# Kernel optimization log

Hardware: AMD Instinct MI355X
Metric: run time of the kernel (lower is better)

Reference implementation:

```python
import jax, jax.numpy as jnp
import numpy as np

N_NODES = 100000
N_EDGES = 3200000
N_GRAPHS = 32
D_IN = 128
D_HID = 128
N_CLASSES = 10


def setup_inputs() -> dict:
    key = jax.random.key(0)
    ks = jax.random.split(key, 16)
    h = jax.random.normal(ks[0], (N_NODES, D_IN), dtype=jnp.float32)
    src = jax.random.randint(ks[1], (N_EDGES,), 0, N_NODES, dtype=jnp.int32)
    dst = jax.random.randint(ks[2], (N_EDGES,), 0, N_NODES, dtype=jnp.int32)
    graph_ids = jnp.sort(jax.random.randint(ks[3], (N_NODES,), 0, N_GRAPHS, dtype=jnp.int32))
    def lin(k, fi, fo):
        s = 1.0 / np.sqrt(fi)
        kw, kb = jax.random.split(k)
        W = jax.random.uniform(kw, (fi, fo), minval=-s, maxval=s, dtype=jnp.float32)
        b = jax.random.uniform(kb, (fo,), minval=-s, maxval=s, dtype=jnp.float32)
        return W, b
    W1, b1 = lin(ks[4], D_IN, D_HID)
    W2, b2 = lin(ks[5], D_HID, D_HID)
    W3, b3 = lin(ks[6], D_HID, D_HID)
    W4, b4 = lin(ks[7], D_HID, D_HID)
    Wc1, bc1 = lin(ks[8], D_HID, D_HID)
    Wc2, bc2 = lin(ks[9], D_HID, N_CLASSES)
    return {"h": h, "src": src, "dst": dst, "graph_ids": graph_ids,
            "W1": W1, "b1": b1, "W2": W2, "b2": b2, "W3": W3, "b3": b3,
            "W4": W4, "b4": b4, "Wc1": Wc1, "bc1": bc1, "Wc2": Wc2, "bc2": bc2}


def _graph_conv(h, src, dst, inv_sqrt_out, inv_sqrt_in, W, b):
    # DGL GraphConv, norm='both': D_dst^{-1/2} A D_src^{-1/2} h W + b
    m = (h * inv_sqrt_out[:, None])[src]            # [E, D] gathered messages
    agg = jax.ops.segment_sum(m, dst, num_segments=h.shape[0])  # [N, D]
    return (agg * inv_sqrt_in[:, None]) @ W + b


def reference(h, src, dst, graph_ids, W1, b1, W2, b2, W3, b3, W4, b4, Wc1, bc1, Wc2, bc2):
    n = h.shape[0]
    ones_e = jnp.ones(src.shape[0], dtype=jnp.float32)
    out_deg = jnp.clip(jax.ops.segment_sum(ones_e, src, num_segments=n), 1.0)
    in_deg = jnp.clip(jax.ops.segment_sum(ones_e, dst, num_segments=n), 1.0)
    inv_sqrt_out = jax.lax.rsqrt(out_deg)
    inv_sqrt_in = jax.lax.rsqrt(in_deg)

    x = jax.nn.relu(_graph_conv(h, src, dst, inv_sqrt_out, inv_sqrt_in, W1, b1))
    x = jax.nn.relu(_graph_conv(x, src, dst, inv_sqrt_out, inv_sqrt_in, W2, b2))
    x = jax.nn.relu(_graph_conv(x, src, dst, inv_sqrt_out, inv_sqrt_in, W3, b3))
    x = jax.nn.relu(_graph_conv(x, src, dst, inv_sqrt_out, inv_sqrt_in, W4, b4))

    # dgl.mean_nodes over batched graphs
    sums = jax.ops.segment_sum(x, graph_ids, num_segments=N_GRAPHS)     # [G, D]
    counts = jax.ops.segment_sum(jnp.ones(n, dtype=jnp.float32), graph_ids, num_segments=N_GRAPHS)
    hg = sums / jnp.clip(counts, 1.0)[:, None]

    out = jax.nn.relu(hg @ Wc1 + bc1)
    out = out @ Wc2 + bc2
    return out
```

## Files before the change

### kernel.cpp

```cpp
#include <hip/hip_runtime.h>

#define D 128
#define NG 32
#define NC 10

typedef unsigned short ushort_t;
typedef __attribute__((ext_vector_type(8))) short short8v;
typedef __attribute__((ext_vector_type(4))) float float4v;

__device__ __forceinline__ ushort_t f2bf(float x) {
  union { float f; unsigned u; } v; v.f = x;
  unsigned r = (v.u + 0x7FFF + ((v.u >> 16) & 1)) >> 16;
  return (ushort_t)r;
}
__device__ __forceinline__ float bf2f(ushort_t b) {
  union { unsigned u; float f; } v; v.u = ((unsigned)b) << 16;
  return v.f;
}

__global__ void degree_kernel(const int* __restrict__ src, const int* __restrict__ dst,
                              int* __restrict__ cout_r, int* __restrict__ cursor,
                              int* __restrict__ rank, int E, int n) {
  int* co = cout_r + (size_t)(blockIdx.x & 3) * n;
  int i = blockIdx.x * 256 + threadIdx.x;
  int e0 = i * 4;
  if (e0 + 4 <= E) {
    int4 s = *(const int4*)(src + e0);
    int4 d_ = *(const int4*)(dst + e0);
    int r0 = atomicAdd(&cursor[d_.x], 1);
    int r1 = atomicAdd(&cursor[d_.y], 1);
    int r2 = atomicAdd(&cursor[d_.z], 1);
    int r3 = atomicAdd(&cursor[d_.w], 1);
    atomicAdd(&co[s.x], 1);
    atomicAdd(&co[s.y], 1);
    atomicAdd(&co[s.z], 1);
    atomicAdd(&co[s.w], 1);
    *(int4*)(rank + e0) = make_int4(r0, r1, r2, r3);
  } else {
    for (int e = e0; e < E; ++e) {
      rank[e] = atomicAdd(&cursor[dst[e]], 1);
      atomicAdd(&co[src[e]], 1);
    }
  }
}

__global__ void sumdeg_kernel(const int* __restrict__ cout_r, int* __restrict__ cout_, int n) {
  int i = blockIdx.x * 256 + threadIdx.x;
  if (i < n)
    cout_[i] = cout_r[i] + cout_r[n + i] + cout_r[2 * (size_t)n + i] + cout_r[3 * (size_t)n + i];
}

__global__ void scan1_kernel(const int* __restrict__ cnt, int* __restrict__ bsum, int n) {
  __shared__ int sdata[256];
  int base = blockIdx.x * 1024 + threadIdx.x * 4;
  int s = 0;
#pragma unroll
  for (int j = 0; j < 4; ++j) {
    int idx = base + j;
    if (idx < n) s += cnt[idx];
  }
  sdata[threadIdx.x] = s;
  __syncthreads();
  for (int off = 128; off > 0; off >>= 1) {
    if (threadIdx.x < off) sdata[threadIdx.x] += sdata[threadIdx.x + off];
    __syncthreads();
  }
  if (threadIdx.x == 0) bsum[blockIdx.x] = sdata[0];
}

__global__ void scan2_kernel(int* __restrict__ bsum, int nb) {
  if (blockIdx.x == 0 && threadIdx.x == 0) {
    int acc = 0;
    for (int i = 0; i < nb; ++i) { int v = bsum[i]; bsum[i] = acc; acc += v; }
  }
}

__global__ void scan3_kernel(const int* __restrict__ cnt, const int* __restrict__ bsum,
                             int* __restrict__ rowptr, int n, int e_total) {
  __shared__ int ss[256];
  int t = threadIdx.x;
  int idx0 = blockIdx.x * 1024 + t * 4;
  int v[4]; int ts = 0;
#pragma unroll
  for (int j = 0; j < 4; ++j) {
    v[j] = (idx0 + j < n) ? cnt[idx0 + j] : 0;
    ts += v[j];
  }
  ss[t] = ts;
  __syncthreads();
  for (int off = 1; off < 256; off <<= 1) {
    int add = 0;
    if (t >= off) add = ss[t - off];
    __syncthreads();
    if (t >= off) ss[t] += add;
    __syncthreads();
  }
  int excl = ss[t] - ts + bsum[blockIdx.x];
#pragma unroll
  for (int j = 0; j < 4; ++j) {
    int idx = idx0 + j;
    if (idx < n) rowptr[idx] = excl;
    excl += v[j];
  }
  if (blockIdx.x == 0 && t == 0) rowptr[n] = e_total;
}

__global__ void passB_kernel(const int* __restrict__ src, const int* __restrict__ dst,
                             const int* __restrict__ rank, const int* __restrict__ rowptr,
                             int* __restrict__ csrc, int E) {
  int i = blockIdx.x * 256 + threadIdx.x;
  int e0 = i * 4;
  if (e0 + 4 <= E) {
    int4 s = *(const int4*)(src + e0);
    int4 d_ = *(const int4*)(dst + e0);
    int4 r = *(const int4*)(rank + e0);
    csrc[rowptr[d_.x] + r.x] = s.x;
    csrc[rowptr[d_.y] + r.y] = s.y;
    csrc[rowptr[d_.z] + r.z] = s.z;
    csrc[rowptr[d_.w] + r.w] = s.w;
  } else {
    for (int e = e0; e < E; ++e)
      csrc[rowptr[dst[e]] + rank[e]] = src[e];
  }
}

__global__ void cvt_h_kernel(const float* __restrict__ h, ushort_t* __restrict__ hb, long total) {
  long i4 = ((long)blockIdx.x * 256 + threadIdx.x) * 4;
  if (i4 + 4 <= total) {
    float4 v = *(const float4*)(h + i4);
    ushort_t o[4] = { f2bf(v.x), f2bf(v.y), f2bf(v.z), f2bf(v.w) };
    *(uint2*)(hb + i4) = *(const uint2*)o;
  } else {
    for (long i = i4; i < total; ++i) hb[i] = f2bf(h[i]);
  }
}

__global__ void cvt_w_kernel(const float* __restrict__ W1, const float* __restrict__ W2,
                             const float* __restrict__ W3, const float* __restrict__ W4,
                             ushort_t* __restrict__ Wt) {
  const float* Ws[4] = { W1, W2, W3, W4 };
  const float* W = Ws[blockIdx.x];
  ushort_t* o = Wt + (size_t)blockIdx.x * D * D;
  for (int idx = threadIdx.x; idx < D * D; idx += 256) {
    int c = idx >> 7, k = idx & 127;
    o[c * D + k] = f2bf(W[k * D + c]);
  }
}

__global__ __launch_bounds__(256) void gemm_mfma_kernel(const ushort_t* __restrict__ A,
    const ushort_t* __restrict__ Wt, const int* __restrict__ cout_,
    ushort_t* __restrict__ X, int n) {
  int wave = threadIdx.x >> 6;
  int lane = threadIdx.x & 63;
  int g = lane >> 4;
  int lr = lane & 15;
  int rowbase = blockIdx.x * 64 + wave * 16;
  int arow = rowbase + lr;
  int arow_c = arow < n ? arow : (n - 1);
  const ushort_t* Ap = A + (size_t)arow_c * D + g * 8;

  short8v afrag[4];
#pragma unroll
  for (int ks = 0; ks < 4; ++ks)
    afrag[ks] = *(const short8v*)(Ap + ks * 32);

  float4v acc[8];
#pragma unroll
  for (int ct = 0; ct < 8; ++ct)
#pragma unroll
    for (int r = 0; r < 4; ++r) acc[ct][r] = 0.f;

#pragma unroll
  for (int ct = 0; ct < 8; ++ct) {
    const ushort_t* bp = Wt + (size_t)(ct * 16 + lr) * D + g * 8;
#pragma unroll
    for (int ks = 0; ks < 4; ++ks) {
      short8v bfrag = *(const short8v*)(bp + ks * 32);
      acc[ct] = __builtin_amdgcn_mfma_f32_16x16x32_bf16(afrag[ks], bfrag, acc[ct], 0, 0, 0);
    }
  }

  float scv[4];
  bool rok[4];
#pragma unroll
  for (int r = 0; r < 4; ++r) {
    int grow = rowbase + g * 4 + r;
    rok[r] = grow < n;
    int gc = rok[r] ? grow : (n - 1);
    scv[r] = rsqrtf(fmaxf((float)cout_[gc], 1.f));
  }
#pragma unroll
  for (int ct = 0; ct < 8; ++ct) {
#pragma unroll
    for (int r = 0; r < 4; ++r) {
      int grow = rowbase + g * 4 + r;
      if (rok[r]) X[(size_t)grow * D + ct * 16 + lr] = f2bf(acc[ct][r] * scv[r]);
    }
  }
}

__global__ __launch_bounds__(256) void agg_relu_kernel(const ushort_t* __restrict__ x,
    const int* __restrict__ rowptr, const int* __restrict__ csrc,
    const int* __restrict__ cin_, const float* __restrict__ bias,
    ushort_t* __restrict__ y, int n) {
  int node = blockIdx.x * 4 + (threadIdx.x >> 6);
  if (node >= n) return;
  int lane = threadIdx.x & 63;
  int beg = rowptr[node], end = rowptr[node + 1];
  float ax = 0.f, ay = 0.f;
  const ushort_t* xp = x + (size_t)(lane * 2);
  int e = beg;
  for (; e + 8 <= end; e += 8) {
    int s[8];
#pragma unroll
    for (int j = 0; j < 8; ++j) s[j] = csrc[e + j];
    ushort2 u[8];
#pragma unroll
    for (int j = 0; j < 8; ++j) u[j] = *(const ushort2*)(xp + (size_t)s[j] * D);
#pragma unroll
    for (int j = 0; j < 8; ++j) { ax += bf2f(u[j].x); ay += bf2f(u[j].y); }
  }
  if (e + 4 <= end) {
    int s[4];
#pragma unroll
    for (int j = 0; j < 4; ++j) s[j] = csrc[e + j];
    ushort2 u[4];
#pragma unroll
    for (int j = 0; j < 4; ++j) u[j] = *(const ushort2*)(xp + (size_t)s[j] * D);
#pragma unroll
    for (int j = 0; j < 4; ++j) { ax += bf2f(u[j].x); ay += bf2f(u[j].y); }
    e += 4;
  }
  for (; e < end; ++e) {
    int s = csrc[e];
    ushort2 u = *(const ushort2*)(xp + (size_t)s * D);
    ax += bf2f(u.x); ay += bf2f(u.y);
  }
  float wi = rsqrtf(fmaxf((float)cin_[node], 1.f));
  float2 bb = *(const float2*)(bias + lane * 2);
  ushort_t o[2] = { f2bf(fmaxf(ax * wi + bb.x, 0.f)), f2bf(fmaxf(ay * wi + bb.y, 0.f)) };
  *(unsigned*)(y + (size_t)node * D + lane * 2) = *(const unsigned*)o;
}

__device__ int lower_bound_gid(const int* gid, int n, int g) {
  int lo = 0, hi = n;
  while (lo < hi) { int mid = (lo + hi) >> 1; if (gid[mid] < g) lo = mid + 1; else hi = mid; }
  return lo;
}

__global__ void pool_kernel(const ushort_t* __restrict__ x, const int* __restrict__ gid,
                            float* __restrict__ sums, int* __restrict__ counts, int n) {
  int g = blockIdx.x >> 3, part = blockIdx.x & 7;
  __shared__ int s_lo, s_hi;
  if (threadIdx.x == 0) {
    s_lo = lower_bound_gid(gid, n, g);
    s_hi = lower_bound_gid(gid, n, g + 1);
    if (part == 0) counts[g] = s_hi - s_lo;
  }
  __syncthreads();
  int lo = s_lo, hi = s_hi;
  int cnt = hi - lo;
  int per = (cnt + 7) >> 3;
  int a = lo + part * per;
  int bnd = min(a + per, hi);
  int t = threadIdx.x;
  float acc = 0.f;
  for (int i = a; i < bnd; ++i) acc += bf2f(x[(size_t)i * D + t]);
  atomicAdd(&sums[g * D + t], acc);
}

__global__ __launch_bounds__(128) void classifier_kernel(const float* __restrict__ sums,
    const int* __restrict__ counts, const float* __restrict__ Wc1, const float* __restrict__ bc1,
    const float* __restrict__ Wc2, const float* __restrict__ bc2, float* __restrict__ out) {
  __shared__ float hg[NG][D];
  __shared__ float hid[NG][D];
  int t = threadIdx.x;
#pragma unroll
  for (int g = 0; g < NG; ++g)
    hg[g][t] = sums[g * D + t] / fmaxf((float)counts[g], 1.f);
  __syncthreads();
  float acc[NG];
#pragma unroll
  for (int g = 0; g < NG; ++g) acc[g] = bc1[t];
  for (int k = 0; k < D; ++k) {
    float w = Wc1[k * D + t];
#pragma unroll
    for (int g = 0; g < NG; ++g) acc[g] += hg[g][k] * w;
  }
#pragma unroll
  for (int g = 0; g < NG; ++g) hid[g][t] = fmaxf(acc[g], 0.f);
  __syncthreads();
  for (int idx = t; idx < NG * NC; idx += 128) {
    int g = idx / NC, c = idx % NC;
    float a = bc2[c];
    for (int j = 0; j < D; ++j) a += hid[g][j] * Wc2[j * NC + c];
    out[idx] = a;
  }
}

extern "C" void kernel_launch(void* const* d_in, const int* in_sizes, int n_in,
                              void* d_out, int out_size, void* d_ws, size_t ws_size,
                              hipStream_t stream) {
  const float* h   = (const float*)d_in[0];
  const int* src   = (const int*)d_in[1];
  const int* dst   = (const int*)d_in[2];
  const int* gid   = (const int*)d_in[3];
  const float* W1  = (const float*)d_in[4];
  const float* b1  = (const float*)d_in[5];
  const float* W2  = (const float*)d_in[6];
  const float* b2  = (const float*)d_in[7];
  const float* W3  = (const float*)d_in[8];
  const float* b3  = (const float*)d_in[9];
  const float* W4  = (const float*)d_in[10];
  const float* b4  = (const float*)d_in[11];
  const float* Wc1 = (const float*)d_in[12];
  const float* bc1 = (const float*)d_in[13];
  const float* Wc2 = (const float*)d_in[14];
  const float* bc2 = (const float*)d_in[15];
  float* out = (float*)d_out;

  const int N = in_sizes[3];
  const int E = in_sizes[1];

  char* ws = (char*)d_ws;
  size_t off = 0;
  auto alloc = [&](size_t bytes) -> char* {
    char* p = ws + off;
    off = (off + bytes + 255) & ~(size_t)255;
    return p;
  };

  int* cnts     = (int*)alloc((size_t)5 * N * 4);
  int* cout_r   = cnts;
  int* cursor   = cnts + (size_t)4 * N;
  int* cout_    = (int*)alloc((size_t)N * 4);
  int* rowptr   = (int*)alloc((size_t)(N + 1) * 4);
  int* bsum     = (int*)alloc(1024);
  int* csrc     = (int*)alloc((size_t)E * 4);
  ushort_t* Wt  = (ushort_t*)alloc((size_t)4 * D * D * 2);
  ushort_t* Xb  = (ushort_t*)alloc((size_t)N * D * 2);
  ushort_t* Yb  = (ushort_t*)alloc((size_t)N * D * 2);
  float* sums   = (float*)alloc((size_t)(NG * D + NG) * 4);
  int* counts   = (int*)(sums + NG * D);
  int* rank     = (int*)Yb;
  ushort_t* Hb  = Yb;

  hipMemsetAsync(cnts, 0, (size_t)5 * N * 4, stream);
  hipMemsetAsync(sums, 0, (size_t)(NG * D + NG) * 4, stream);

  int gE4 = (E / 4 + 255) / 256 + 1;
  int gN  = (N + 255) / 256;
  int nb  = (N + 1023) / 1024;
  int gAgg  = (N + 3) / 4;
  int gGemm = (N + 63) / 64;
  long totalH = (long)N * D;
  int gCvt = (int)((totalH / 4 + 255) / 256) + 1;

  degree_kernel<<<gE4, 256, 0, stream>>>(src, dst, cout_r, cursor, rank, E, N);
  sumdeg_kernel<<<gN, 256, 0, stream>>>(cout_r, cout_, N);
  scan1_kernel<<<nb, 256, 0, stream>>>(cursor, bsum, N);
  scan2_kernel<<<1, 64, 0, stream>>>(bsum, nb);
  scan3_kernel<<<nb, 256, 0, stream>>>(cursor, bsum, rowptr, N, E);
  passB_kernel<<<gE4, 256, 0, stream>>>(src, dst, rank, rowptr, csrc, E);

  cvt_w_kernel<<<4, 256, 0, stream>>>(W1, W2, W3, W4, Wt);
  cvt_h_kernel<<<gCvt, 256, 0, stream>>>(h, Hb, totalH);

  gemm_mfma_kernel<<<gGemm, 256, 0, stream>>>(Hb, Wt, cout_, Xb, N);
  agg_relu_kernel<<<gAgg, 256, 0, stream>>>(Xb, rowptr, csrc, cursor, b1, Yb, N);
  gemm_mfma_kernel<<<gGemm, 256, 0, stream>>>(Yb, Wt + (size_t)1 * D * D, cout_, Xb, N);
  agg_relu_kernel<<<gAgg, 256, 0, stream>>>(Xb, rowptr, csrc, cursor, b2, Yb, N);
  gemm_mfma_kernel<<<gGemm, 256, 0, stream>>>(Yb, Wt + (size_t)2 * D * D, cout_, Xb, N);
  agg_relu_kernel<<<gAgg, 256, 0, stream>>>(Xb, rowptr, csrc, cursor, b3, Yb, N);
  gemm_mfma_kernel<<<gGemm, 256, 0, stream>>>(Yb, Wt + (size_t)3 * D * D, cout_, Xb, N);
  agg_relu_kernel<<<gAgg, 256, 0, stream>>>(Xb, rowptr, csrc, cursor, b4, Yb, N);

  pool_kernel<<<NG * 8, 128, 0, stream>>>(Yb, gid, sums, counts, N);
  classifier_kernel<<<1, 128, 0, stream>>>(sums, counts, Wc1, bc1, Wc2, bc2, out);
}
```

Before: 1.076 ms.

## Store GEMM output in FP8 for aggregation gathers; drop replicated out-degree counters

The GEMM output that the aggregation kernel gathers per edge is now stored as FP8 (e4m3 via the packed convert builtin) instead of bf16. This halves the bytes each edge gather reads and shrinks the gathered buffer so more of it fits in cache. The out-degree counting also goes back to a single array of atomics, which removes the sumdeg kernel and the 4x replicated counters but adds atomic contention. FP8 lowers precision a lot and may hurt accuracy against the float32 reference.

Result: faster. 955.8 us (-11.1%).

```diff
diff --git a/kernel.cpp b/kernel.cpp
--- a/kernel.cpp
+++ b/kernel.cpp
@@ -7,6 +7,7 @@
 typedef unsigned short ushort_t;
 typedef __attribute__((ext_vector_type(8))) short short8v;
 typedef __attribute__((ext_vector_type(4))) float float4v;
+typedef __attribute__((ext_vector_type(2))) float float2v;
 
 __device__ __forceinline__ ushort_t f2bf(float x) {
   union { float f; unsigned u; } v; v.f = x;
@@ -19,9 +20,8 @@
 }
 
 __global__ void degree_kernel(const int* __restrict__ src, const int* __restrict__ dst,
-                              int* __restrict__ cout_r, int* __restrict__ cursor,
-                              int* __restrict__ rank, int E, int n) {
-  int* co = cout_r + (size_t)(blockIdx.x & 3) * n;
+                              int* __restrict__ cout_, int* __restrict__ cursor,
+                              int* __restrict__ rank, int E) {
   int i = blockIdx.x * 256 + threadIdx.x;
   int e0 = i * 4;
   if (e0 + 4 <= E) {
@@ -31,23 +31,17 @@
     int r1 = atomicAdd(&cursor[d_.y], 1);
     int r2 = atomicAdd(&cursor[d_.z], 1);
     int r3 = atomicAdd(&cursor[d_.w], 1);
-    atomicAdd(&co[s.x], 1);
-    atomicAdd(&co[s.y], 1);
-    atomicAdd(&co[s.z], 1);
-    atomicAdd(&co[s.w], 1);
+    atomicAdd(&cout_[s.x], 1);
+    atomicAdd(&cout_[s.y], 1);
+    atomicAdd(&cout_[s.z], 1);
+    atomicAdd(&cout_[s.w], 1);
     *(int4*)(rank + e0) = make_int4(r0, r1, r2, r3);
   } else {
     for (int e = e0; e < E; ++e) {
       rank[e] = atomicAdd(&cursor[dst[e]], 1);
-      atomicAdd(&co[src[e]], 1);
-    }
-  }
-}
-
-__global__ void sumdeg_kernel(const int* __restrict__ cout_r, int* __restrict__ cout_, int n) {
-  int i = blockIdx.x * 256 + threadIdx.x;
-  if (i < n)
-    cout_[i] = cout_r[i] + cout_r[n + i] + cout_r[2 * (size_t)n + i] + cout_r[3 * (size_t)n + i];
+      atomicAdd(&cout_[src[e]], 1);
+    }
+  }
 }
 
 __global__ void scan1_kernel(const int* __restrict__ cnt, int* __restrict__ bsum, int n) {
@@ -149,7 +143,7 @@
 
 __global__ __launch_bounds__(256) void gemm_mfma_kernel(const ushort_t* __restrict__ A,
     const ushort_t* __restrict__ Wt, const int* __restrict__ cout_,
-    ushort_t* __restrict__ X, int n) {
+    unsigned char* __restrict__ X, int n) {
   int wave = threadIdx.x >> 6;
   int lane = threadIdx.x & 63;
   int g = lane >> 4;
@@ -194,12 +188,15 @@
 #pragma unroll
     for (int r = 0; r < 4; ++r) {
       int grow = rowbase + g * 4 + r;
-      if (rok[r]) X[(size_t)grow * D + ct * 16 + lr] = f2bf(acc[ct][r] * scv[r]);
-    }
-  }
-}
-
-__global__ __launch_bounds__(256) void agg_relu_kernel(const ushort_t* __restrict__ x,
+      if (rok[r]) {
+        int p = __builtin_amdgcn_cvt_pk_fp8_f32(acc[ct][r] * scv[r], 0.f, 0, false);
+        X[(size_t)grow * D + ct * 16 + lr] = (unsigned char)(p & 0xff);
+      }
+    }
+  }
+}
+
+__global__ __launch_bounds__(256) void agg_relu_kernel(const unsigned char* __restrict__ x,
     const int* __restrict__ rowptr, const int* __restrict__ csrc,
     const int* __restrict__ cin_, const float* __restrict__ bias,
     ushort_t* __restrict__ y, int n) {
@@ -208,33 +205,40 @@
   int lane = threadIdx.x & 63;
   int beg = rowptr[node], end = rowptr[node + 1];
   float ax = 0.f, ay = 0.f;
-  const ushort_t* xp = x + (size_t)(lane * 2);
+  const unsigned char* xp = x + lane * 2;
   int e = beg;
   for (; e + 8 <= end; e += 8) {
     int s[8];
 #pragma unroll
     for (int j = 0; j < 8; ++j) s[j] = csrc[e + j];
-    ushort2 u[8];
-#pragma unroll
-    for (int j = 0; j < 8; ++j) u[j] = *(const ushort2*)(xp + (size_t)s[j] * D);
-#pragma unroll
-    for (int j = 0; j < 8; ++j) { ax += bf2f(u[j].x); ay += bf2f(u[j].y); }
+    ushort_t u[8];
+#pragma unroll
+    for (int j = 0; j < 8; ++j) u[j] = *(const ushort_t*)(xp + (size_t)s[j] * D);
+#pragma unroll
+    for (int j = 0; j < 8; ++j) {
+      float2v f = __builtin_amdgcn_cvt_pk_f32_fp8((unsigned)u[j], false);
+      ax += f[0]; ay += f[1];
+    }
   }
   if (e + 4 <= end) {
     int s[4];
 #pragma unroll
     for (int j = 0; j < 4; ++j) s[j] = csrc[e + j];
-    ushort2 u[4];
-#pragma unroll
-    for (int j = 0; j < 4; ++j) u[j] = *(const ushort2*)(xp + (size_t)s[j] * D);
-#pragma unroll
-    for (int j = 0; j < 4; ++j) { ax += bf2f(u[j].x); ay += bf2f(u[j].y); }
+    ushort_t u[4];
+#pragma unroll
+    for (int j = 0; j < 4; ++j) u[j] = *(const ushort_t*)(xp + (size_t)s[j] * D);
+#pragma unroll
+    for (int j = 0; j < 4; ++j) {
+      float2v f = __builtin_amdgcn_cvt_pk_f32_fp8((unsigned)u[j], false);
+      ax += f[0]; ay += f[1];
+    }
     e += 4;
   }
   for (; e < end; ++e) {
     int s = csrc[e];
-    ushort2 u = *(const ushort2*)(xp + (size_t)s * D);
-    ax += bf2f(u.x); ay += bf2f(u.y);
+    ushort_t u = *(const ushort_t*)(xp + (size_t)s * D);
+    float2v f = __builtin_amdgcn_cvt_pk_f32_fp8((unsigned)u, false);
+    ax += f[0]; ay += f[1];
   }
   float wi = rsqrtf(fmaxf((float)cin_[node], 1.f));
   float2 bb = *(const float2*)(bias + lane * 2);
@@ -330,34 +334,31 @@
     return p;
   };
 
-  int* cnts     = (int*)alloc((size_t)5 * N * 4);
-  int* cout_r   = cnts;
-  int* cursor   = cnts + (size_t)4 * N;
-  int* cout_    = (int*)alloc((size_t)N * 4);
+  int* cnts     = (int*)alloc((size_t)2 * N * 4);
+  int* cout_    = cnts;
+  int* cursor   = cnts + N;
   int* rowptr   = (int*)alloc((size_t)(N + 1) * 4);
   int* bsum     = (int*)alloc(1024);
   int* csrc     = (int*)alloc((size_t)E * 4);
   ushort_t* Wt  = (ushort_t*)alloc((size_t)4 * D * D * 2);
-  ushort_t* Xb  = (ushort_t*)alloc((size_t)N * D * 2);
+  unsigned char* Xb = (unsigned char*)alloc((size_t)N * D);
   ushort_t* Yb  = (ushort_t*)alloc((size_t)N * D * 2);
   float* sums   = (float*)alloc((size_t)(NG * D + NG) * 4);
   int* counts   = (int*)(sums + NG * D);
   int* rank     = (int*)Yb;
   ushort_t* Hb  = Yb;
 
-  hipMemsetAsync(cnts, 0, (size_t)5 * N * 4, stream);
+  hipMemsetAsync(cnts, 0, (size_t)2 * N * 4, stream);
   hipMemsetAsync(sums, 0, (size_t)(NG * D + NG) * 4, stream);
 
   int gE4 = (E / 4 + 255) / 256 + 1;
-  int gN  = (N + 255) / 256;
   int nb  = (N + 1023) / 1024;
   int gAgg  = (N + 3) / 4;
   int gGemm = (N + 63) / 64;
   long totalH = (long)N * D;
   int gCvt = (int)((totalH / 4 + 255) / 256) + 1;
 
-  degree_kernel<<<gE4, 256, 0, stream>>>(src, dst, cout_r, cursor, rank, E, N);
-  sumdeg_kernel<<<gN, 256, 0, stream>>>(cout_r, cout_, N);
+  degree_kernel<<<gE4, 256, 0, stream>>>(src, dst, cout_, cursor, rank, E);
   scan1_kernel<<<nb, 256, 0, stream>>>(cursor, bsum, N);
   scan2_kernel<<<1, 64, 0, stream>>>(bsum, nb);
   scan3_kernel<<<nb, 256, 0, stream>>>(cursor, bsum, rowptr, N, E);
```
